# Kernel tuning notes

Hardware: AMD Instinct MI355X
Metric: run time of the kernel (lower is better)

## Reference

```python
import jax, jax.numpy as jnp
import numpy as np

B_SZ, SEQ_LEN, D_MODEL, STATE_SIZE = 2, 2048, 1024, 16


def setup_inputs() -> dict:
    key = jax.random.key(0)
    ks = jax.random.split(key, 5)
    d, n = D_MODEL, STATE_SIZE
    x = jax.random.normal(ks[0], (B_SZ, SEQ_LEN, d), dtype=jnp.float32)
    # torch Linear weights are [out_features, in_features]
    W1 = jax.random.normal(ks[1], (d, d), dtype=jnp.float32) * (1.0 / np.sqrt(d))
    b1 = jnp.zeros((d,), dtype=jnp.float32)
    W2 = jax.random.normal(ks[2], (n, d), dtype=jnp.float32) * (1.0 / np.sqrt(d))
    b2 = jnp.zeros((n,), dtype=jnp.float32)
    W3 = jax.random.normal(ks[3], (n, d), dtype=jnp.float32) * (1.0 / np.sqrt(d))
    b3 = jnp.zeros((n,), dtype=jnp.float32)
    A = jax.random.normal(ks[4], (d, n), dtype=jnp.float32) * 0.3  # xavier-ish init
    return {"x": x, "W1": W1, "b1": b1, "W2": W2, "b2": b2, "W3": W3, "b3": b3, "A": A}


def reference(x, W1, b1, W2, b2, W3, b3, A):
    # B, C: [b, l, n]; delta: [b, l, d]
    Bm = jnp.einsum('bld,nd->bln', x, W2) + b2
    Cm = jnp.einsum('bld,nd->bln', x, W3) + b3
    delta = jax.nn.softplus(jnp.einsum('bld,ed->ble', x, W1) + b1)
    # discretization: dB, dA are [b, l, d, n]
    dB = jnp.einsum('bld,bln->bldn', delta, Bm)
    dA = jnp.exp(jnp.einsum('bld,dn->bldn', delta, A))
    # initial hidden state is zeros, so the dA*h term vanishes (kept for fidelity)
    h0 = jnp.zeros_like(dB)
    h = dA * h0 + x[..., None] * dB  # [b, l, d, n]
    y = jnp.einsum('bln,bldn->bld', Cm, h)
    return y
```

## Files before the change

kernel.cpp:

```cpp
#include <hip/hip_runtime.h>
#include <hip/hip_bf16.h>


#define ROWS 4096
#define KDIM 1024
#define BM 128
#define BN 64
#define BK 32

typedef __attribute__((ext_vector_type(8))) __bf16 bf16x8;
typedef __attribute__((ext_vector_type(4))) float f32x4;

__device__ __forceinline__ unsigned short f2bf_rne(float f) {
    unsigned u = __float_as_uint(f);
    u += 0x7FFFu + ((u >> 16) & 1u);
    return (unsigned short)(u >> 16);
}
__device__ __forceinline__ unsigned pack2(float lo, float hi) {
    return (unsigned)f2bf_rne(lo) | ((unsigned)f2bf_rne(hi) << 16);
}
__device__ __forceinline__ void async16(const void* g, void* l) {
    __builtin_amdgcn_global_load_lds(
        (const __attribute__((address_space(1))) void*)g,
        (__attribute__((address_space(3))) void*)l, 16, 0, 0);
}

__global__ __launch_bounds__(256) void prep_kernel(
        const float* __restrict__ x,  const float* __restrict__ W1,
        const float* __restrict__ W2, const float* __restrict__ W3,
        unsigned short* __restrict__ xb, unsigned short* __restrict__ w1b,
        unsigned short* __restrict__ w2b, unsigned short* __restrict__ w3b) {
    const long long NX  = (long long)ROWS * KDIM;
    const long long NW1 = (long long)KDIM * KDIM;
    const long long NW  = 16LL * KDIM;
    long long i = ((long long)blockIdx.x * 256 + threadIdx.x) * 8;
    const float* src;
    unsigned short* dst;
    if (i < NX)                 { src = x  + i;                 dst = xb  + i; }
    else if (i < NX + NW1)      { src = W1 + (i - NX);          dst = w1b + (i - NX); }
    else if (i < NX + NW1 + NW) { src = W2 + (i - NX - NW1);    dst = w2b + (i - NX - NW1); }
    else                        { src = W3 + (i - NX - NW1 - NW); dst = w3b + (i - NX - NW1 - NW); }
    float4 a = *(const float4*)src;
    float4 b = *(const float4*)(src + 4);
    uint4 o;
    o.x = pack2(a.x, a.y); o.y = pack2(a.z, a.w);
    o.z = pack2(b.x, b.y); o.w = pack2(b.z, b.w);
    *(uint4*)dst = o;
}

__global__ __launch_bounds__(256) void s_kernel(
        const unsigned short* __restrict__ xb,
        const unsigned short* __restrict__ w2b, const float* __restrict__ b2,
        const unsigned short* __restrict__ w3b, const float* __restrict__ b3,
        float* __restrict__ s) {
    __shared__ f32x4 redB[4][64];
    __shared__ f32x4 redC[4][64];
    const int t = threadIdx.x;
    const int lane = t & 63;
    const int wv = t >> 6;
    const int m = lane & 15;
    const int kq = (lane >> 4) * 8;
    const int r0 = blockIdx.x * 16;
    const int kbase = wv * 256;

    f32x4 accB = (f32x4){0.f, 0.f, 0.f, 0.f};
    f32x4 accC = (f32x4){0.f, 0.f, 0.f, 0.f};
    const unsigned short* xr  = xb  + (size_t)(r0 + m) * KDIM + kbase + kq;
    const unsigned short* w2r = w2b + (size_t)m * KDIM + kbase + kq;
    const unsigned short* w3r = w3b + (size_t)m * KDIM + kbase + kq;
#pragma unroll
    for (int ks = 0; ks < 256; ks += 32) {
        bf16x8 af  = *(const bf16x8*)(xr  + ks);
        bf16x8 b2f = *(const bf16x8*)(w2r + ks);
        bf16x8 b3f = *(const bf16x8*)(w3r + ks);
        accB = __builtin_amdgcn_mfma_f32_16x16x32_bf16(af, b2f, accB, 0, 0, 0);
        accC = __builtin_amdgcn_mfma_f32_16x16x32_bf16(af, b3f, accC, 0, 0, 0);
    }
    redB[wv][lane] = accB;
    redC[wv][lane] = accC;
    __syncthreads();
    if (wv == 0) {
        f32x4 tB = redB[0][lane], tC = redC[0][lane];
#pragma unroll
        for (int w = 1; w < 4; ++w) { tB += redB[w][lane]; tC += redC[w][lane]; }
        const float b2n = b2[m], b3n = b3[m];
        const int q4 = (lane >> 4) * 4;
#pragma unroll
        for (int r = 0; r < 4; ++r) {
            float p = (tB[r] + b2n) * (tC[r] + b3n);
            p += __shfl_xor(p, 1, 64);
            p += __shfl_xor(p, 2, 64);
            p += __shfl_xor(p, 4, 64);
            p += __shfl_xor(p, 8, 64);
            if (m == 0) s[r0 + q4 + r] = p;
        }
    }
}

__global__ __launch_bounds__(256) void gemm_fused(
        const unsigned short* __restrict__ xb,
        const unsigned short* __restrict__ w1b,
        const float* __restrict__ b1,
        const float* __restrict__ x,
        const float* __restrict__ s,
        float* __restrict__ y) {
    __shared__ __align__(16) unsigned short As[BM * BK];
    __shared__ __align__(16) unsigned short Bs[BN * BK];

    const int bid = blockIdx.x;
    const int xcd = bid & 7;
    const int l = bid >> 3;
    const int row0 = (xcd * 4 + (l >> 4)) * BM;
    const int col0 = (l & 15) * BN;

    const int t = threadIdx.x;
    const int lane = t & 63;
    const int wv = t >> 6;
    const int wm = wv >> 1;
    const int wn = wv & 1;

    f32x4 acc[4][2];
#pragma unroll
    for (int mi = 0; mi < 4; ++mi)
#pragma unroll
        for (int ni = 0; ni < 2; ++ni)
            acc[mi][ni] = (f32x4){0.f, 0.f, 0.f, 0.f};

    const int srow = (lane >> 2);
    const int skoff = (lane & 3) * 8;
    const int ml = lane & 15;
    const int kq = (lane >> 4) * 8;

    for (int k0 = 0; k0 < KDIM; k0 += BK) {
        __syncthreads();
#pragma unroll
        for (int i = 0; i < 2; ++i) {
            int c = wv * 2 + i;
            int rrow = c * 16 + srow;
            async16(xb + (size_t)(row0 + rrow) * KDIM + k0 + skoff, &As[c * 512]);
        }
        {
            int rrow = wv * 16 + srow;
            async16(w1b + (size_t)(col0 + rrow) * KDIM + k0 + skoff, &Bs[wv * 512]);
        }
        __syncthreads();

        bf16x8 af[4], bfr[2];
#pragma unroll
        for (int i = 0; i < 4; ++i)
            af[i]  = *(const bf16x8*)&As[(wm * 64 + i * 16 + ml) * BK + kq];
#pragma unroll
        for (int i = 0; i < 2; ++i)
            bfr[i] = *(const bf16x8*)&Bs[(wn * 32 + i * 16 + ml) * BK + kq];
#pragma unroll
        for (int mi = 0; mi < 4; ++mi)
#pragma unroll
            for (int ni = 0; ni < 2; ++ni)
                acc[mi][ni] = __builtin_amdgcn_mfma_f32_16x16x32_bf16(
                    af[mi], bfr[ni], acc[mi][ni], 0, 0, 0);
    }

    const int q4 = (lane >> 4) * 4;
#pragma unroll
    for (int mi = 0; mi < 4; ++mi) {
        const int rbase = row0 + wm * 64 + mi * 16 + q4;
        float4 s4 = *(const float4*)&s[rbase];
        const float* sp4 = (const float*)&s4;
#pragma unroll
        for (int ni = 0; ni < 2; ++ni) {
            const int c = col0 + wn * 32 + ni * 16 + ml;
            const float bias = b1[c];
#pragma unroll
            for (int r = 0; r < 4; ++r) {
                float z = acc[mi][ni][r] + bias;
                float sp = fmaxf(z, 0.f) + log1pf(__expf(-fabsf(z)));
                size_t idx = (size_t)(rbase + r) * KDIM + c;
                y[idx] = sp * x[idx] * sp4[r];
            }
        }
    }
}

extern "C" void kernel_launch(void* const* d_in, const int* in_sizes, int n_in,
                              void* d_out, int out_size, void* d_ws, size_t ws_size,
                              hipStream_t stream) {
    const float* x  = (const float*)d_in[0];
    const float* W1 = (const float*)d_in[1];
    const float* b1 = (const float*)d_in[2];
    const float* W2 = (const float*)d_in[3];
    const float* b2 = (const float*)d_in[4];
    const float* W3 = (const float*)d_in[5];
    const float* b3 = (const float*)d_in[6];
    float* y = (float*)d_out;

    unsigned short* xb  = (unsigned short*)d_ws;
    unsigned short* w1b = xb  + (size_t)ROWS * KDIM;
    unsigned short* w2b = w1b + (size_t)KDIM * KDIM;
    unsigned short* w3b = w2b + (size_t)16 * KDIM;
    float* s = (float*)(w3b + (size_t)16 * KDIM);

    prep_kernel<<<dim3(2576), dim3(256), 0, stream>>>(x, W1, W2, W3, xb, w1b, w2b, w3b);
    s_kernel<<<dim3(256), dim3(256), 0, stream>>>(xb, w2b, b2, w3b, b3, s);
    gemm_fused<<<dim3(512), dim3(256), 0, stream>>>(xb, w1b, b1, x, s, y);
}
```

Before: 121.8 us.

## Load GEMM fragments directly from global memory, dropping LDS staging

The fused GEMM no longer stages A and B tiles through shared memory with async global-to-LDS loads and two barriers per k-step. Each wave now reads its MFMA operand fragments straight from global memory, relying on L1/L2 for the reuse between waves, with the k loop unrolled by four so more loads can be in flight. Occupancy is hinted at two blocks per CU. This removes barrier and LDS overhead but issues more global traffic per block, since operand rows are fetched separately by each wave.

```diff
diff --git a/kernel.cpp b/kernel.cpp
--- a/kernel.cpp
+++ b/kernel.cpp
@@ -4,9 +4,6 @@
 
 #define ROWS 4096
 #define KDIM 1024
-#define BM 128
-#define BN 64
-#define BK 32
 
 typedef __attribute__((ext_vector_type(8))) __bf16 bf16x8;
 typedef __attribute__((ext_vector_type(4))) float f32x4;
@@ -18,11 +15,6 @@
 }
 __device__ __forceinline__ unsigned pack2(float lo, float hi) {
     return (unsigned)f2bf_rne(lo) | ((unsigned)f2bf_rne(hi) << 16);
-}
-__device__ __forceinline__ void async16(const void* g, void* l) {
-    __builtin_amdgcn_global_load_lds(
-        (const __attribute__((address_space(1))) void*)g,
-        (__attribute__((address_space(3))) void*)l, 16, 0, 0);
 }
 
 __global__ __launch_bounds__(256) void prep_kernel(
@@ -97,27 +89,26 @@
     }
 }
 
-__global__ __launch_bounds__(256) void gemm_fused(
+__global__ __launch_bounds__(256, 2) void gemm_fused(
         const unsigned short* __restrict__ xb,
         const unsigned short* __restrict__ w1b,
         const float* __restrict__ b1,
         const float* __restrict__ x,
         const float* __restrict__ s,
         float* __restrict__ y) {
-    __shared__ __align__(16) unsigned short As[BM * BK];
-    __shared__ __align__(16) unsigned short Bs[BN * BK];
-
     const int bid = blockIdx.x;
     const int xcd = bid & 7;
     const int l = bid >> 3;
-    const int row0 = (xcd * 4 + (l >> 4)) * BM;
-    const int col0 = (l & 15) * BN;
+    const int row0 = (xcd * 4 + (l >> 4)) * 128;
+    const int col0 = (l & 15) * 64;
 
     const int t = threadIdx.x;
     const int lane = t & 63;
     const int wv = t >> 6;
     const int wm = wv >> 1;
     const int wn = wv & 1;
+    const int m = lane & 15;
+    const int kq = (lane >> 4) * 8;
 
     f32x4 acc[4][2];
 #pragma unroll
@@ -126,32 +117,18 @@
         for (int ni = 0; ni < 2; ++ni)
             acc[mi][ni] = (f32x4){0.f, 0.f, 0.f, 0.f};
 
-    const int srow = (lane >> 2);
-    const int skoff = (lane & 3) * 8;
-    const int ml = lane & 15;
-    const int kq = (lane >> 4) * 8;
+    const unsigned short* pa = xb  + (size_t)(row0 + wm * 64 + m) * KDIM + kq;
+    const unsigned short* pb = w1b + (size_t)(col0 + wn * 32 + m) * KDIM + kq;
 
-    for (int k0 = 0; k0 < KDIM; k0 += BK) {
-        __syncthreads();
-#pragma unroll
-        for (int i = 0; i < 2; ++i) {
-            int c = wv * 2 + i;
-            int rrow = c * 16 + srow;
-            async16(xb + (size_t)(row0 + rrow) * KDIM + k0 + skoff, &As[c * 512]);
-        }
-        {
-            int rrow = wv * 16 + srow;
-            async16(w1b + (size_t)(col0 + rrow) * KDIM + k0 + skoff, &Bs[wv * 512]);
-        }
-        __syncthreads();
-
+#pragma unroll 4
+    for (int k0 = 0; k0 < KDIM; k0 += 32) {
         bf16x8 af[4], bfr[2];
 #pragma unroll
         for (int i = 0; i < 4; ++i)
-            af[i]  = *(const bf16x8*)&As[(wm * 64 + i * 16 + ml) * BK + kq];
+            af[i] = *(const bf16x8*)(pa + (size_t)i * 16 * KDIM + k0);
 #pragma unroll
         for (int i = 0; i < 2; ++i)
-            bfr[i] = *(const bf16x8*)&Bs[(wn * 32 + i * 16 + ml) * BK + kq];
+            bfr[i] = *(const bf16x8*)(pb + (size_t)i * 16 * KDIM + k0);
 #pragma unroll
         for (int mi = 0; mi < 4; ++mi)
 #pragma unroll
@@ -168,7 +145,7 @@
         const float* sp4 = (const float*)&s4;
 #pragma unroll
         for (int ni = 0; ni < 2; ++ni) {
-            const int c = col0 + wn * 32 + ni * 16 + ml;
+            const int c = col0 + wn * 32 + ni * 16 + m;
             const float bias = b1[c];
 #pragma unroll
             for (int r = 0; r < 4; ++r) {
```

New measurement: 146.6 us. 20.4% more time.
